# Kernel optimization log

Measured on AMD Instinct MI355X. Metric: run time of the kernel, lower is better.

## Reference

```python
import jax, jax.numpy as jnp
import numpy as np

DIM = 1024
HEADS = 16
DIM_HEAD = 64
INNER = HEADS * DIM_HEAD  # 1024
FF_INNER = 4 * DIM        # 4096
EPS = 1e-5


def _ln(t, gamma):
    mu = jnp.mean(t, axis=-1, keepdims=True)
    var = jnp.var(t, axis=-1, keepdims=True)
    return (t - mu) * jax.lax.rsqrt(var + EPS) * gamma


def setup_inputs() -> dict:
    key = jax.random.key(0)
    ks = jax.random.split(key, 8)
    B, N = 4, 1024
    s = 0.02
    return {
        "x": jax.random.normal(ks[0], (B, N, DIM), dtype=jnp.float32),
        "y": jax.random.normal(ks[1], (B, N, DIM), dtype=jnp.float32),
        "g1": jnp.ones((DIM,), dtype=jnp.float32),
        "g2": jnp.ones((DIM,), dtype=jnp.float32),
        "g_out": jnp.ones((DIM,), dtype=jnp.float32),
        "Wq": jax.random.normal(ks[2], (DIM, INNER), dtype=jnp.float32) * s,
        "Wkv": jax.random.normal(ks[3], (DIM, 2 * DIM_HEAD), dtype=jnp.float32) * s,
        "Wo": jax.random.normal(ks[4], (INNER, DIM), dtype=jnp.float32) * s,
        "Wff1": jax.random.normal(ks[5], (DIM, 2 * FF_INNER), dtype=jnp.float32) * s,
        "Wff2": jax.random.normal(ks[6], (FF_INNER, DIM), dtype=jnp.float32) * s,
    }


def reference(x, y, g1, g2, g_out, Wq, Wkv, Wo, Wff1, Wff2):
    B, N, _ = x.shape
    scale = DIM_HEAD ** -0.5
    xn = _ln(x, g1)
    yn = _ln(y, g2)  # note: torch code rebinds y = norm2(y); residual & FF use normed y
    # multi-query attention: per-head queries, single shared k/v head
    q = (xn @ Wq).reshape(B, N, HEADS, DIM_HEAD).transpose(0, 2, 1, 3) * scale  # b h n d
    kv = yn @ Wkv  # b j (2d)
    k, v = kv[..., :DIM_HEAD], kv[..., DIM_HEAD:]
    sim = jnp.einsum('bhid,bjd->bhij', q, k)
    attn = jax.nn.softmax(sim, axis=-1)  # torch code subtracts amax then softmax; identical math
    out = jnp.einsum('bhij,bjd->bhid', attn, v)
    out = out.transpose(0, 2, 1, 3).reshape(B, N, INNER)
    out = out @ Wo
    out = _ln(out + yn, g_out)
    # SwiGLU FFN on normed y: first half is value, second half is gate
    h = yn @ Wff1
    val, gate = h[..., :FF_INNER], h[..., FF_INNER:]
    ff = (jax.nn.silu(gate) * val) @ Wff2
    return out + ff
```

## Files before the change

kernel.cpp:

```cpp
#include <hip/hip_runtime.h>
#include <hip/hip_bf16.h>


typedef __attribute__((ext_vector_type(8))) short bf16x8;
typedef __attribute__((ext_vector_type(4))) short s16x4;
typedef __attribute__((ext_vector_type(4))) float f32x4;

__device__ __forceinline__ short f2b(float f) {
  union { float f; unsigned u; } v; v.f = f;
  unsigned r = (v.u + 0x7fffu + ((v.u >> 16) & 1u)) >> 16;
  return (short)r;
}

__device__ __forceinline__ void gload16(const short* g, short* l) {
  __builtin_amdgcn_global_load_lds(
      (const __attribute__((address_space(1))) void*)g,
      (__attribute__((address_space(3))) void*)l, 16, 0, 0);
}

__global__ __launch_bounds__(256) void cvtT_kernel(const float* __restrict__ in,
                                                   short* __restrict__ out,
                                                   int K, int N) {
  __shared__ float tile[32][33];
  int n0 = blockIdx.x * 32, k0 = blockIdx.y * 32;
  int tx = threadIdx.x & 7, ty = threadIdx.x >> 3;
  float4 v = *(const float4*)&in[(size_t)(k0 + ty) * N + n0 + tx * 4];
  tile[ty][tx * 4 + 0] = v.x;
  tile[ty][tx * 4 + 1] = v.y;
  tile[ty][tx * 4 + 2] = v.z;
  tile[ty][tx * 4 + 3] = v.w;
  __syncthreads();
  s16x4 o = { f2b(tile[tx * 4 + 0][ty]), f2b(tile[tx * 4 + 1][ty]),
              f2b(tile[tx * 4 + 2][ty]), f2b(tile[tx * 4 + 3][ty]) };
  *(s16x4*)&out[(size_t)(n0 + ty) * K + k0 + tx * 4] = o;
}

__global__ __launch_bounds__(256) void ln_kernel(const float* __restrict__ in,
                                                 const float* __restrict__ gamma,
                                                 short* __restrict__ out16,
                                                 float* __restrict__ out32) {
  int row = blockIdx.x;
  int t = threadIdx.x;
  float4 v = ((const float4*)(in + (size_t)row * 1024))[t];
  float s  = v.x + v.y + v.z + v.w;
  float sq = v.x*v.x + v.y*v.y + v.z*v.z + v.w*v.w;
  __shared__ float ssum[256], ssq[256];
  ssum[t] = s; ssq[t] = sq;
  __syncthreads();
  for (int o = 128; o > 0; o >>= 1) {
    if (t < o) { ssum[t] += ssum[t + o]; ssq[t] += ssq[t + o]; }
    __syncthreads();
  }
  float mu  = ssum[0] * (1.0f / 1024.0f);
  float var = ssq[0] * (1.0f / 1024.0f) - mu * mu;
  float rs  = rsqrtf(var + 1e-5f);
  float4 g = ((const float4*)gamma)[t];
  float o0 = (v.x - mu) * rs * g.x;
  float o1 = (v.y - mu) * rs * g.y;
  float o2 = (v.z - mu) * rs * g.z;
  float o3 = (v.w - mu) * rs * g.w;
  if (out16) {
    s16x4 o = { f2b(o0), f2b(o1), f2b(o2), f2b(o3) };
    ((s16x4*)out16)[(size_t)row * 256 + t] = o;
  }
  if (out32) {
    float4 o = { o0, o1, o2, o3 };
    ((float4*)out32)[(size_t)row * 256 + t] = o;
  }
}

template<int EPI, bool DUAL, int BM, int BN>
__global__ __launch_bounds__(256, 2) void gemm_ring(
    const short* __restrict__ A, const short* __restrict__ B,
    int M, int N, int Kstride, int Klen,
    short* __restrict__ out16, float* __restrict__ out32,
    const float* __restrict__ res, float scale)
{
  constexpr int DEPTH = DUAL ? 3 : 4;
  constexpr int FM = BM / 32;
  constexpr int FN = BN / 32;
  constexpr int AL = BM / 64;
  constexpr int BL = BN / 64;
  constexpr int LPT = AL + BL * (DUAL ? 2 : 1);
  __shared__ __align__(16) short As[DEPTH][BM * 32];
  __shared__ __align__(16) short Bs[DEPTH][BN * 32];
  __shared__ __align__(16) short Bs2[DUAL ? DEPTH : 1][DUAL ? BN * 32 : 8];

  int t = threadIdx.x;
  int lane = t & 63, wave = t >> 6;
  int wm = wave >> 1, wn = wave & 1;
  int lrow = lane & 15, lgrp = lane >> 4;
  int m0 = blockIdx.y * BM, n0 = blockIdx.x * BN;
  int kbase = blockIdx.z * Klen;

  int srow = lane >> 2, scol = (lane & 3) * 8;
  const short* gA  = A + (size_t)(m0 + wave * 16 + srow) * Kstride + kbase + scol;
  const short* gB  = B + (size_t)(n0 + wave * 16 + srow) * Kstride + kbase + scol;
  const short* gB2 = DUAL ? B + (size_t)(4096 + n0 + wave * 16 + srow) * Kstride + kbase + scol : gB;

  auto STAGE = [&](int slot, int kt) {
    int k0 = kt * 32;
#pragma unroll
    for (int i = 0; i < AL; i++)
      gload16(gA + (size_t)(i * 64) * Kstride + k0, &As[slot][(i * 4 + wave) * 512]);
#pragma unroll
    for (int j = 0; j < BL; j++)
      gload16(gB + (size_t)(j * 64) * Kstride + k0, &Bs[slot][(j * 4 + wave) * 512]);
    if constexpr (DUAL) {
#pragma unroll
      for (int j = 0; j < BL; j++)
        gload16(gB2 + (size_t)(j * 64) * Kstride + k0, &Bs2[slot][(j * 4 + wave) * 512]);
    }
  };

  f32x4 acc[FM][FN];
  f32x4 acc2[DUAL ? FM : 1][DUAL ? FN : 1];
  const f32x4 zero = { 0.f, 0.f, 0.f, 0.f };
#pragma unroll
  for (int i = 0; i < FM; i++)
#pragma unroll
    for (int j = 0; j < FN; j++) { acc[i][j] = zero; if (DUAL) acc2[i][j] = zero; }

  int nt = Klen / 32;
#pragma unroll
  for (int p = 0; p < DEPTH - 1; p++) STAGE(p, p);

  int slot = 0, stage_slot = DEPTH - 1;
  for (int tI = 0; tI < nt; ++tI) {
    int rem = nt - 1 - tI;
    if constexpr (DUAL) {
      if (rem >= 1) asm volatile("s_waitcnt vmcnt(6)" ::: "memory");
      else          asm volatile("s_waitcnt vmcnt(0)" ::: "memory");
    } else if constexpr (LPT == 4) {
      if (rem >= 2)      asm volatile("s_waitcnt vmcnt(8)" ::: "memory");
      else if (rem == 1) asm volatile("s_waitcnt vmcnt(4)" ::: "memory");
      else               asm volatile("s_waitcnt vmcnt(0)" ::: "memory");
    } else {
      if (rem >= 2)      asm volatile("s_waitcnt vmcnt(6)" ::: "memory");
      else if (rem == 1) asm volatile("s_waitcnt vmcnt(3)" ::: "memory");
      else               asm volatile("s_waitcnt vmcnt(0)" ::: "memory");
    }
    __builtin_amdgcn_s_barrier();
    __builtin_amdgcn_sched_barrier(0);

    if (tI + DEPTH - 1 < nt) STAGE(stage_slot, tI + DEPTH - 1);

    bf16x8 af[FM], bfr[FN], bfr2[DUAL ? FN : 1];
#pragma unroll
    for (int mf = 0; mf < FM; mf++)
      af[mf] = *(const bf16x8*)&As[slot][(wm * (BM / 2) + mf * 16 + lrow) * 32 + lgrp * 8];
#pragma unroll
    for (int nf = 0; nf < FN; nf++)
      bfr[nf] = *(const bf16x8*)&Bs[slot][(wn * (BN / 2) + nf * 16 + lrow) * 32 + lgrp * 8];
    if constexpr (DUAL) {
#pragma unroll
      for (int nf = 0; nf < FN; nf++)
        bfr2[nf] = *(const bf16x8*)&Bs2[slot][(wn * (BN / 2) + nf * 16 + lrow) * 32 + lgrp * 8];
    }

    __builtin_amdgcn_s_setprio(1);
#pragma unroll
    for (int mf = 0; mf < FM; mf++)
#pragma unroll
      for (int nf = 0; nf < FN; nf++) {
        acc[mf][nf] = __builtin_amdgcn_mfma_f32_16x16x32_bf16(af[mf], bfr[nf], acc[mf][nf], 0, 0, 0);
        if constexpr (DUAL)
          acc2[mf][nf] = __builtin_amdgcn_mfma_f32_16x16x32_bf16(af[mf], bfr2[nf], acc2[mf][nf], 0, 0, 0);
      }
    __builtin_amdgcn_s_setprio(0);

    slot = (slot + 1 == DEPTH) ? 0 : slot + 1;
    stage_slot = (stage_slot + 1 == DEPTH) ? 0 : stage_slot + 1;
  }

#pragma unroll
  for (int mf = 0; mf < FM; mf++)
#pragma unroll
    for (int nf = 0; nf < FN; nf++)
#pragma unroll
      for (int r = 0; r < 4; r++) {
        int row = m0 + wm * (BM / 2) + mf * 16 + lgrp * 4 + r;
        int col = n0 + wn * (BN / 2) + nf * 16 + lrow;
        float v = acc[mf][nf][r];
        if (EPI == 0) {
          out16[(size_t)row * N + col] = f2b(v * scale);
        } else if (EPI == 1) {
          out32[(size_t)row * N + col] = v + res[(size_t)row * N + col];
        } else if (EPI == 3) {
          out32[(size_t)blockIdx.z * M * N + (size_t)row * N + col] = v;
        } else {
          float gate = acc2[mf][nf][r];
          float sig = 1.0f / (1.0f + __expf(-gate));
          out16[(size_t)row * N + col] = f2b(v * gate * sig);
        }
      }
}

__global__ __launch_bounds__(256) void kvred_kernel(const float* __restrict__ p,
                                                    short* __restrict__ out, int n4) {
  int i = blockIdx.x * 256 + threadIdx.x;
  if (i >= n4) return;
  const int S = 4096 * 128 / 4;
  float4 a = ((const float4*)p)[i];
  float4 b = ((const float4*)p)[i + S];
  float4 c = ((const float4*)p)[i + 2 * S];
  float4 d = ((const float4*)p)[i + 3 * S];
  s16x4 o = { f2b(a.x + b.x + c.x + d.x), f2b(a.y + b.y + c.y + d.y),
              f2b(a.z + b.z + c.z + d.z), f2b(a.w + b.w + c.w + d.w) };
  ((s16x4*)out)[i] = o;
}

__global__ __launch_bounds__(256) void attn_kernel(const short* __restrict__ q,
                                                   const short* __restrict__ kv,
                                                   short* __restrict__ ao)
{
  __shared__ __align__(16) short Ks[64 * 64];
  __shared__ __align__(16) short Vs[64 * 64];
  __shared__ __align__(16) short Ps[4][32 * 64];

  int t = threadIdx.x;
  int lane = t & 63, wave = t >> 6;
  int lrow = lane & 15, lgrp = lane >> 4;
  int qt = blockIdx.x;
  int b = blockIdx.y >> 2, hg = blockIdx.y & 3;
  int h = hg * 4 + wave;

  char* Kb = (char*)Ks;
  char* Vb = (char*)Vs;
  char* Pb = (char*)Ps + wave * (32 * 64 * 2);

  bf16x8 qf[2][2];
  const short* qb = q + ((size_t)(b * 1024 + qt * 32)) * 1024 + h * 64;
#pragma unroll
  for (int mf = 0; mf < 2; mf++)
#pragma unroll
    for (int kk = 0; kk < 2; kk++)
      qf[mf][kk] = *(const bf16x8*)&qb[(size_t)(mf * 16 + lrow) * 1024 + kk * 32 + lgrp * 8];

  f32x4 oacc[2][4];
  float m_[2][4], l_[2][4];
  const f32x4 zero = { 0.f, 0.f, 0.f, 0.f };
#pragma unroll
  for (int i = 0; i < 2; i++)
#pragma unroll
    for (int j = 0; j < 4; j++) { oacc[i][j] = zero; }
#pragma unroll
  for (int i = 0; i < 2; i++)
#pragma unroll
    for (int r = 0; r < 4; r++) { m_[i][r] = -3.0e38f; l_[i][r] = 0.f; }

  int4 d[4];
  {
    const short* kvb = kv + ((size_t)(b * 1024 + lane)) * 128 + wave * 32;
#pragma unroll
    for (int i = 0; i < 4; i++) d[i] = ((const int4*)kvb)[i];
  }

  for (int j0 = 0; j0 < 1024; j0 += 64) {
    __syncthreads();
    if (wave < 2) {
      int sw = (lane & 7) << 4;
#pragma unroll
      for (int i = 0; i < 4; i++)
        *(int4*)(Kb + lane * 128 + ((wave * 64 + i * 16) ^ sw)) = d[i];
    } else {
#pragma unroll
      for (int i = 0; i < 4; i++) {
        union { int4 v; short s[8]; } u; u.v = d[i];
#pragma unroll
        for (int j = 0; j < 8; j++) {
          int dd = (wave - 2) * 32 + i * 8 + j;
          *(short*)(Vb + dd * 128 + ((lane * 2) ^ ((dd & 7) << 4))) = u.s[j];
        }
      }
    }
    if (j0 + 64 < 1024) {
      const short* kvn = kv + ((size_t)(b * 1024 + j0 + 64 + lane)) * 128 + wave * 32;
#pragma unroll
      for (int i = 0; i < 4; i++) d[i] = ((const int4*)kvn)[i];
    }
    __syncthreads();

    bf16x8 kf[4][2];
#pragma unroll
    for (int nf = 0; nf < 4; nf++) {
      int row = nf * 16 + lrow, sw = (row & 7) << 4;
      kf[nf][0] = *(const bf16x8*)(Kb + row * 128 + ((lgrp * 16) ^ sw));
      kf[nf][1] = *(const bf16x8*)(Kb + row * 128 + ((64 + lgrp * 16) ^ sw));
    }
    f32x4 sacc[2][4];
#pragma unroll
    for (int i = 0; i < 2; i++)
#pragma unroll
      for (int j = 0; j < 4; j++) sacc[i][j] = zero;
    __builtin_amdgcn_s_setprio(1);
#pragma unroll
    for (int mf = 0; mf < 2; mf++)
#pragma unroll
      for (int nf = 0; nf < 4; nf++)
#pragma unroll
        for (int kk = 0; kk < 2; kk++)
          sacc[mf][nf] = __builtin_amdgcn_mfma_f32_16x16x32_bf16(qf[mf][kk], kf[nf][kk], sacc[mf][nf], 0, 0, 0);
    __builtin_amdgcn_s_setprio(0);

    float pmax[2][4];
    bool okd = true;
#pragma unroll
    for (int mf = 0; mf < 2; mf++)
#pragma unroll
      for (int r = 0; r < 4; r++) {
        float pm = fmaxf(fmaxf(sacc[mf][0][r], sacc[mf][1][r]),
                         fmaxf(sacc[mf][2][r], sacc[mf][3][r]));
        pmax[mf][r] = pm;
        okd = okd && (pm <= m_[mf][r] + 8.0f);
      }
    if (__all(okd)) {
#pragma unroll
      for (int mf = 0; mf < 2; mf++)
#pragma unroll
        for (int r = 0; r < 4; r++) {
          int row = mf * 16 + lgrp * 4 + r, sw = (row & 7) << 4;
          float al = 0.f;
#pragma unroll
          for (int nf = 0; nf < 4; nf++) {
            float p = __expf(sacc[mf][nf][r] - m_[mf][r]);
            *(short*)(Pb + row * 128 + (((nf * 16 + lrow) * 2) ^ sw)) = f2b(p);
            al += p;
          }
          l_[mf][r] += al;
        }
    } else {
#pragma unroll
      for (int mf = 0; mf < 2; mf++)
#pragma unroll
        for (int r = 0; r < 4; r++) {
          float mx = pmax[mf][r];
#pragma unroll
          for (int o = 8; o >= 1; o >>= 1) mx = fmaxf(mx, __shfl_xor(mx, o));
          float mnew = fmaxf(m_[mf][r], mx);
          float corr = __expf(m_[mf][r] - mnew);
          int row = mf * 16 + lgrp * 4 + r, sw = (row & 7) << 4;
          float al = 0.f;
#pragma unroll
          for (int nf = 0; nf < 4; nf++) {
            float p = __expf(sacc[mf][nf][r] - mnew);
            *(short*)(Pb + row * 128 + (((nf * 16 + lrow) * 2) ^ sw)) = f2b(p);
            al += p;
          }
          l_[mf][r] = l_[mf][r] * corr + al;
          m_[mf][r] = mnew;
#pragma unroll
          for (int nf = 0; nf < 4; nf++) oacc[mf][nf][r] *= corr;
        }
    }

    bf16x8 vf[4][2], pf[2][2];
#pragma unroll
    for (int nf = 0; nf < 4; nf++) {
      int row = nf * 16 + lrow, sw = (row & 7) << 4;
      vf[nf][0] = *(const bf16x8*)(Vb + row * 128 + ((lgrp * 16) ^ sw));
      vf[nf][1] = *(const bf16x8*)(Vb + row * 128 + ((64 + lgrp * 16) ^ sw));
    }
#pragma unroll
    for (int mf = 0; mf < 2; mf++) {
      int row = mf * 16 + lrow, sw = (row & 7) << 4;
      pf[mf][0] = *(const bf16x8*)(Pb + row * 128 + ((lgrp * 16) ^ sw));
      pf[mf][1] = *(const bf16x8*)(Pb + row * 128 + ((64 + lgrp * 16) ^ sw));
    }
    __builtin_amdgcn_s_setprio(1);
#pragma unroll
    for (int mf = 0; mf < 2; mf++)
#pragma unroll
      for (int nf = 0; nf < 4; nf++)
#pragma unroll
        for (int kk = 0; kk < 2; kk++)
          oacc[mf][nf] = __builtin_amdgcn_mfma_f32_16x16x32_bf16(pf[mf][kk], vf[nf][kk], oacc[mf][nf], 0, 0, 0);
    __builtin_amdgcn_s_setprio(0);
  }

#pragma unroll
  for (int mf = 0; mf < 2; mf++)
#pragma unroll
    for (int r = 0; r < 4; r++) {
      float ls = l_[mf][r];
#pragma unroll
      for (int o = 8; o >= 1; o >>= 1) ls += __shfl_xor(ls, o);
      float inv = 1.0f / ls;
      int qrow = qt * 32 + mf * 16 + lgrp * 4 + r;
#pragma unroll
      for (int nf = 0; nf < 4; nf++) {
        float val = oacc[mf][nf][r] * inv;
        ao[((size_t)(b * 1024 + qrow)) * 1024 + h * 64 + nf * 16 + lrow] = f2b(val);
      }
    }
}

extern "C" void kernel_launch(void* const* d_in, const int* in_sizes, int n_in,
                              void* d_out, int out_size, void* d_ws, size_t ws_size,
                              hipStream_t stream) {
  const float* x     = (const float*)d_in[0];
  const float* y     = (const float*)d_in[1];
  const float* g1    = (const float*)d_in[2];
  const float* g2    = (const float*)d_in[3];
  const float* g_out = (const float*)d_in[4];
  const float* Wq    = (const float*)d_in[5];
  const float* Wkv   = (const float*)d_in[6];
  const float* Wo    = (const float*)d_in[7];
  const float* Wff1  = (const float*)d_in[8];
  const float* Wff2  = (const float*)d_in[9];

  char* ws = (char*)d_ws;
  size_t off = 0;
  auto alloc = [&](size_t bytes) { char* p = ws + off; off += bytes; return p; };
  short* wqT    = (short*)alloc((size_t)1024 * 1024 * 2);
  short* wkvT   = (short*)alloc((size_t)128 * 1024 * 2);
  short* woT    = (short*)alloc((size_t)1024 * 1024 * 2);
  short* wff1T  = (short*)alloc((size_t)8192 * 1024 * 2);
  short* wff2T  = (short*)alloc((size_t)1024 * 4096 * 2);
  short* xn16   = (short*)alloc((size_t)4096 * 1024 * 2);
  short* yn16   = (short*)alloc((size_t)4096 * 1024 * 2);
  float* ynf    = (float*)alloc((size_t)4096 * 1024 * 4);
  short* q16    = (short*)alloc((size_t)4096 * 1024 * 2);
  short* kv16   = (short*)alloc((size_t)4096 * 128 * 2);
  short* ao16   = (short*)alloc((size_t)4096 * 1024 * 2);
  float* lnout  = (float*)alloc((size_t)4096 * 1024 * 4);
  short* act16  = (short*)alloc((size_t)4096 * 4096 * 2);
  float* kvpart = (float*)alloc((size_t)4 * 4096 * 128 * 4);
  float* outf   = (float*)d_out;

  cvtT_kernel<<<dim3(1024 / 32, 1024 / 32), 256, 0, stream>>>(Wq,   wqT,   1024, 1024);
  cvtT_kernel<<<dim3(128 / 32, 1024 / 32),  256, 0, stream>>>(Wkv,  wkvT,  1024, 128);
  cvtT_kernel<<<dim3(1024 / 32, 1024 / 32), 256, 0, stream>>>(Wo,   woT,   1024, 1024);
  cvtT_kernel<<<dim3(8192 / 32, 1024 / 32), 256, 0, stream>>>(Wff1, wff1T, 1024, 8192);
  cvtT_kernel<<<dim3(1024 / 32, 4096 / 32), 256, 0, stream>>>(Wff2, wff2T, 4096, 1024);

  ln_kernel<<<4096, 256, 0, stream>>>(x, g1, xn16, nullptr);
  ln_kernel<<<4096, 256, 0, stream>>>(y, g2, yn16, ynf);

  gemm_ring<0, false, 64, 128><<<dim3(8, 64), 256, 0, stream>>>(
      xn16, wqT, 4096, 1024, 1024, 1024, q16, nullptr, nullptr, 0.125f);
  gemm_ring<3, false, 64, 128><<<dim3(1, 64, 4), 256, 0, stream>>>(
      yn16, wkvT, 4096, 128, 1024, 256, nullptr, kvpart, nullptr, 1.0f);
  kvred_kernel<<<512, 256, 0, stream>>>(kvpart, kv16, 4096 * 128 / 4);

  attn_kernel<<<dim3(32, 16), 256, 0, stream>>>(q16, kv16, ao16);

  gemm_ring<1, false, 64, 128><<<dim3(8, 64), 256, 0, stream>>>(
      ao16, woT, 4096, 1024, 1024, 1024, nullptr, outf, ynf, 1.0f);

  ln_kernel<<<4096, 256, 0, stream>>>(outf, g_out, nullptr, lnout);

  gemm_ring<2, true, 128, 128><<<dim3(32, 32), 256, 0, stream>>>(
      yn16, wff1T, 4096, 4096, 1024, 1024, act16, nullptr, nullptr, 1.0f);

  gemm_ring<1, false, 64, 128><<<dim3(8, 64), 256, 0, stream>>>(
      act16, wff2T, 4096, 1024, 4096, 4096, nullptr, outf, lnout, 1.0f);
}
```

Before: 325.4 us.

## Add dedicated 8-wave SwiGLU FF1 GEMM with interleaved prefetch phases

Replaces the dual-B templated GEMM path for the SwiGLU FF1 projection with a dedicated kernel. It uses 512 threads, a 256x128 tile with separate value and gate B buffers, and a 4-deep ring. Each k-step is split into four barrier-separated MFMA phases, with global-to-LDS prefetches spread across the phases to overlap loads with compute. The dual path is removed from the generic GEMM template. The extra barriers add synchronization overhead, and the larger tile and accumulator count raise register pressure.

New measurement: 324.6 us. About the same (-0.3%).

```diff
diff --git a/kernel.cpp b/kernel.cpp
--- a/kernel.cpp
+++ b/kernel.cpp
@@ -69,22 +69,20 @@
   }
 }
 
-template<int EPI, bool DUAL, int BM, int BN>
+template<int EPI, int BM, int BN>
 __global__ __launch_bounds__(256, 2) void gemm_ring(
     const short* __restrict__ A, const short* __restrict__ B,
     int M, int N, int Kstride, int Klen,
     short* __restrict__ out16, float* __restrict__ out32,
     const float* __restrict__ res, float scale)
 {
-  constexpr int DEPTH = DUAL ? 3 : 4;
+  constexpr int DEPTH = 4;
   constexpr int FM = BM / 32;
   constexpr int FN = BN / 32;
   constexpr int AL = BM / 64;
   constexpr int BL = BN / 64;
-  constexpr int LPT = AL + BL * (DUAL ? 2 : 1);
   __shared__ __align__(16) short As[DEPTH][BM * 32];
   __shared__ __align__(16) short Bs[DEPTH][BN * 32];
-  __shared__ __align__(16) short Bs2[DUAL ? DEPTH : 1][DUAL ? BN * 32 : 8];
 
   int t = threadIdx.x;
   int lane = t & 63, wave = t >> 6;
@@ -94,9 +92,8 @@
   int kbase = blockIdx.z * Klen;
 
   int srow = lane >> 2, scol = (lane & 3) * 8;
-  const short* gA  = A + (size_t)(m0 + wave * 16 + srow) * Kstride + kbase + scol;
-  const short* gB  = B + (size_t)(n0 + wave * 16 + srow) * Kstride + kbase + scol;
-  const short* gB2 = DUAL ? B + (size_t)(4096 + n0 + wave * 16 + srow) * Kstride + kbase + scol : gB;
+  const short* gA = A + (size_t)(m0 + wave * 16 + srow) * Kstride + kbase + scol;
+  const short* gB = B + (size_t)(n0 + wave * 16 + srow) * Kstride + kbase + scol;
 
   auto STAGE = [&](int slot, int kt) {
     int k0 = kt * 32;
@@ -106,20 +103,14 @@
 #pragma unroll
     for (int j = 0; j < BL; j++)
       gload16(gB + (size_t)(j * 64) * Kstride + k0, &Bs[slot][(j * 4 + wave) * 512]);
-    if constexpr (DUAL) {
-#pragma unroll
-      for (int j = 0; j < BL; j++)
-        gload16(gB2 + (size_t)(j * 64) * Kstride + k0, &Bs2[slot][(j * 4 + wave) * 512]);
-    }
   };
 
   f32x4 acc[FM][FN];
-  f32x4 acc2[DUAL ? FM : 1][DUAL ? FN : 1];
   const f32x4 zero = { 0.f, 0.f, 0.f, 0.f };
 #pragma unroll
   for (int i = 0; i < FM; i++)
 #pragma unroll
-    for (int j = 0; j < FN; j++) { acc[i][j] = zero; if (DUAL) acc2[i][j] = zero; }
+    for (int j = 0; j < FN; j++) acc[i][j] = zero;
 
   int nt = Klen / 32;
 #pragma unroll
@@ -128,10 +119,7 @@
   int slot = 0, stage_slot = DEPTH - 1;
   for (int tI = 0; tI < nt; ++tI) {
     int rem = nt - 1 - tI;
-    if constexpr (DUAL) {
-      if (rem >= 1) asm volatile("s_waitcnt vmcnt(6)" ::: "memory");
-      else          asm volatile("s_waitcnt vmcnt(0)" ::: "memory");
-    } else if constexpr (LPT == 4) {
+    if constexpr (AL + BL == 4) {
       if (rem >= 2)      asm volatile("s_waitcnt vmcnt(8)" ::: "memory");
       else if (rem == 1) asm volatile("s_waitcnt vmcnt(4)" ::: "memory");
       else               asm volatile("s_waitcnt vmcnt(0)" ::: "memory");
@@ -145,28 +133,20 @@
 
     if (tI + DEPTH - 1 < nt) STAGE(stage_slot, tI + DEPTH - 1);
 
-    bf16x8 af[FM], bfr[FN], bfr2[DUAL ? FN : 1];
+    bf16x8 af[FM], bfr[FN];
 #pragma unroll
     for (int mf = 0; mf < FM; mf++)
       af[mf] = *(const bf16x8*)&As[slot][(wm * (BM / 2) + mf * 16 + lrow) * 32 + lgrp * 8];
 #pragma unroll
     for (int nf = 0; nf < FN; nf++)
       bfr[nf] = *(const bf16x8*)&Bs[slot][(wn * (BN / 2) + nf * 16 + lrow) * 32 + lgrp * 8];
-    if constexpr (DUAL) {
+
+    __builtin_amdgcn_s_setprio(1);
+#pragma unroll
+    for (int mf = 0; mf < FM; mf++)
 #pragma unroll
       for (int nf = 0; nf < FN; nf++)
-        bfr2[nf] = *(const bf16x8*)&Bs2[slot][(wn * (BN / 2) + nf * 16 + lrow) * 32 + lgrp * 8];
-    }
-
-    __builtin_amdgcn_s_setprio(1);
-#pragma unroll
-    for (int mf = 0; mf < FM; mf++)
-#pragma unroll
-      for (int nf = 0; nf < FN; nf++) {
         acc[mf][nf] = __builtin_amdgcn_mfma_f32_16x16x32_bf16(af[mf], bfr[nf], acc[mf][nf], 0, 0, 0);
-        if constexpr (DUAL)
-          acc2[mf][nf] = __builtin_amdgcn_mfma_f32_16x16x32_bf16(af[mf], bfr2[nf], acc2[mf][nf], 0, 0, 0);
-      }
     __builtin_amdgcn_s_setprio(0);
 
     slot = (slot + 1 == DEPTH) ? 0 : slot + 1;
@@ -186,13 +166,132 @@
           out16[(size_t)row * N + col] = f2b(v * scale);
         } else if (EPI == 1) {
           out32[(size_t)row * N + col] = v + res[(size_t)row * N + col];
-        } else if (EPI == 3) {
+        } else {
           out32[(size_t)blockIdx.z * M * N + (size_t)row * N + col] = v;
-        } else {
-          float gate = acc2[mf][nf][r];
-          float sig = 1.0f / (1.0f + __expf(-gate));
-          out16[(size_t)row * N + col] = f2b(v * gate * sig);
         }
+      }
+}
+
+__global__ __launch_bounds__(512, 2) void gemm_ff1(
+    const short* __restrict__ A, const short* __restrict__ B,
+    short* __restrict__ out16)
+{
+  constexpr int K = 1024, NT = 32;
+  __shared__ __align__(16) short As[4][256 * 32];
+  __shared__ __align__(16) short Bv[4][128 * 32];
+  __shared__ __align__(16) short Bg[4][128 * 32];
+
+  int t = threadIdx.x;
+  int lane = t & 63, wave = t >> 6;
+  int wm = wave >> 1, wn = wave & 1;
+  int lrow = lane & 15, lgrp = lane >> 4;
+  int m0 = blockIdx.y * 256, n0 = blockIdx.x * 128;
+
+  int srow = lane >> 2, scol = (lane & 3) * 8;
+  const short* gA  = A + (size_t)(m0 + wave * 16 + srow) * K + scol;
+  const short* gBv = B + (size_t)(n0 + wave * 16 + srow) * K + scol;
+  const short* gBg = B + (size_t)(4096 + n0 + wave * 16 + srow) * K + scol;
+
+  f32x4 acc[4][4], acc2[4][4];
+  const f32x4 zero = { 0.f, 0.f, 0.f, 0.f };
+#pragma unroll
+  for (int i = 0; i < 4; i++)
+#pragma unroll
+    for (int j = 0; j < 4; j++) { acc[i][j] = zero; acc2[i][j] = zero; }
+
+#pragma unroll
+  for (int p = 0; p < 3; p++) {
+    gload16(gA + p * 32,                      &As[p][wave * 512]);
+    gload16(gA + (size_t)128 * K + p * 32,    &As[p][4096 + wave * 512]);
+    gload16(gBv + p * 32,                     &Bv[p][wave * 512]);
+    gload16(gBg + p * 32,                     &Bg[p][wave * 512]);
+  }
+
+  for (int tI = 0; tI < NT; ++tI) {
+    int slot = tI & 3, s3 = (tI + 3) & 3;
+    bool pf = (tI + 3 < NT);
+    int k3 = (tI + 3) * 32;
+    int rem = NT - 1 - tI;
+    if (rem >= 2)      asm volatile("s_waitcnt vmcnt(8)" ::: "memory");
+    else if (rem == 1) asm volatile("s_waitcnt vmcnt(4)" ::: "memory");
+    else               asm volatile("s_waitcnt vmcnt(0)" ::: "memory");
+    __builtin_amdgcn_s_barrier();
+    __builtin_amdgcn_sched_barrier(0);
+
+    bf16x8 af[4], bv[4], bg[4];
+#pragma unroll
+    for (int mf = 0; mf < 4; mf++)
+      af[mf] = *(const bf16x8*)&As[slot][(wm * 64 + mf * 16 + lrow) * 32 + lgrp * 8];
+    bv[0] = *(const bf16x8*)&Bv[slot][(wn * 64 + lrow) * 32 + lgrp * 8];
+    bv[1] = *(const bf16x8*)&Bv[slot][(wn * 64 + 16 + lrow) * 32 + lgrp * 8];
+    if (pf) gload16(gA + k3, &As[s3][wave * 512]);
+    __builtin_amdgcn_s_barrier();
+    __builtin_amdgcn_sched_barrier(0);
+    __builtin_amdgcn_s_setprio(1);
+#pragma unroll
+    for (int mf = 0; mf < 4; mf++) {
+      acc[mf][0] = __builtin_amdgcn_mfma_f32_16x16x32_bf16(af[mf], bv[0], acc[mf][0], 0, 0, 0);
+      acc[mf][1] = __builtin_amdgcn_mfma_f32_16x16x32_bf16(af[mf], bv[1], acc[mf][1], 0, 0, 0);
+    }
+    __builtin_amdgcn_s_setprio(0);
+    __builtin_amdgcn_s_barrier();
+    __builtin_amdgcn_sched_barrier(0);
+    bv[2] = *(const bf16x8*)&Bv[slot][(wn * 64 + 32 + lrow) * 32 + lgrp * 8];
+    bv[3] = *(const bf16x8*)&Bv[slot][(wn * 64 + 48 + lrow) * 32 + lgrp * 8];
+    if (pf) gload16(gA + (size_t)128 * K + k3, &As[s3][4096 + wave * 512]);
+    __builtin_amdgcn_s_barrier();
+    __builtin_amdgcn_sched_barrier(0);
+    __builtin_amdgcn_s_setprio(1);
+#pragma unroll
+    for (int mf = 0; mf < 4; mf++) {
+      acc[mf][2] = __builtin_amdgcn_mfma_f32_16x16x32_bf16(af[mf], bv[2], acc[mf][2], 0, 0, 0);
+      acc[mf][3] = __builtin_amdgcn_mfma_f32_16x16x32_bf16(af[mf], bv[3], acc[mf][3], 0, 0, 0);
+    }
+    __builtin_amdgcn_s_setprio(0);
+    __builtin_amdgcn_s_barrier();
+    __builtin_amdgcn_sched_barrier(0);
+    bg[0] = *(const bf16x8*)&Bg[slot][(wn * 64 + lrow) * 32 + lgrp * 8];
+    bg[1] = *(const bf16x8*)&Bg[slot][(wn * 64 + 16 + lrow) * 32 + lgrp * 8];
+    if (pf) gload16(gBv + k3, &Bv[s3][wave * 512]);
+    __builtin_amdgcn_s_barrier();
+    __builtin_amdgcn_sched_barrier(0);
+    __builtin_amdgcn_s_setprio(1);
+#pragma unroll
+    for (int mf = 0; mf < 4; mf++) {
+      acc2[mf][0] = __builtin_amdgcn_mfma_f32_16x16x32_bf16(af[mf], bg[0], acc2[mf][0], 0, 0, 0);
+      acc2[mf][1] = __builtin_amdgcn_mfma_f32_16x16x32_bf16(af[mf], bg[1], acc2[mf][1], 0, 0, 0);
+    }
+    __builtin_amdgcn_s_setprio(0);
+    __builtin_amdgcn_s_barrier();
+    __builtin_amdgcn_sched_barrier(0);
+    bg[2] = *(const bf16x8*)&Bg[slot][(wn * 64 + 32 + lrow) * 32 + lgrp * 8];
+    bg[3] = *(const bf16x8*)&Bg[slot][(wn * 64 + 48 + lrow) * 32 + lgrp * 8];
+    if (pf) gload16(gBg + k3, &Bg[s3][wave * 512]);
+    __builtin_amdgcn_s_barrier();
+    __builtin_amdgcn_sched_barrier(0);
+    __builtin_amdgcn_s_setprio(1);
+#pragma unroll
+    for (int mf = 0; mf < 4; mf++) {
+      acc2[mf][2] = __builtin_amdgcn_mfma_f32_16x16x32_bf16(af[mf], bg[2], acc2[mf][2], 0, 0, 0);
+      acc2[mf][3] = __builtin_amdgcn_mfma_f32_16x16x32_bf16(af[mf], bg[3], acc2[mf][3], 0, 0, 0);
+    }
+    __builtin_amdgcn_s_setprio(0);
+    __builtin_amdgcn_s_barrier();
+    __builtin_amdgcn_sched_barrier(0);
+  }
+
+#pragma unroll
+  for (int mf = 0; mf < 4; mf++)
+#pragma unroll
+    for (int nf = 0; nf < 4; nf++)
+#pragma unroll
+      for (int r = 0; r < 4; r++) {
+        int row = m0 + wm * 64 + mf * 16 + lgrp * 4 + r;
+        int col = n0 + wn * 64 + nf * 16 + lrow;
+        float v = acc[mf][nf][r];
+        float gate = acc2[mf][nf][r];
+        float sig = 1.0f / (1.0f + __expf(-gate));
+        out16[(size_t)row * 4096 + col] = f2b(v * gate * sig);
       }
 }
 
@@ -354,7 +453,7 @@
         }
     }
 
-    bf16x8 vf[4][2], pf[2][2];
+    bf16x8 vf[4][2], pfr[2][2];
 #pragma unroll
     for (int nf = 0; nf < 4; nf++) {
       int row = nf * 16 + lrow, sw = (row & 7) << 4;
@@ -364,8 +463,8 @@
 #pragma unroll
     for (int mf = 0; mf < 2; mf++) {
       int row = mf * 16 + lrow, sw = (row & 7) << 4;
-      pf[mf][0] = *(const bf16x8*)(Pb + row * 128 + ((lgrp * 16) ^ sw));
-      pf[mf][1] = *(const bf16x8*)(Pb + row * 128 + ((64 + lgrp * 16) ^ sw));
+      pfr[mf][0] = *(const bf16x8*)(Pb + row * 128 + ((lgrp * 16) ^ sw));
+      pfr[mf][1] = *(const bf16x8*)(Pb + row * 128 + ((64 + lgrp * 16) ^ sw));
     }
     __builtin_amdgcn_s_setprio(1);
 #pragma unroll
@@ -374,7 +473,7 @@
       for (int nf = 0; nf < 4; nf++)
 #pragma unroll
         for (int kk = 0; kk < 2; kk++)
-          oacc[mf][nf] = __builtin_amdgcn_mfma_f32_16x16x32_bf16(pf[mf][kk], vf[nf][kk], oacc[mf][nf], 0, 0, 0);
+          oacc[mf][nf] = __builtin_amdgcn_mfma_f32_16x16x32_bf16(pfr[mf][kk], vf[nf][kk], oacc[mf][nf], 0, 0, 0);
     __builtin_amdgcn_s_setprio(0);
   }
 
@@ -437,22 +536,21 @@
   ln_kernel<<<4096, 256, 0, stream>>>(x, g1, xn16, nullptr);
   ln_kernel<<<4096, 256, 0, stream>>>(y, g2, yn16, ynf);
 
-  gemm_ring<0, false, 64, 128><<<dim3(8, 64), 256, 0, stream>>>(
+  gemm_ring<0, 64, 128><<<dim3(8, 64), 256, 0, stream>>>(
       xn16, wqT, 4096, 1024, 1024, 1024, q16, nullptr, nullptr, 0.125f);
-  gemm_ring<3, false, 64, 128><<<dim3(1, 64, 4), 256, 0, stream>>>(
+  gemm_ring<3, 64, 128><<<dim3(1, 64, 4), 256, 0, stream>>>(
       yn16, wkvT, 4096, 128, 1024, 256, nullptr, kvpart, nullptr, 1.0f);
   kvred_kernel<<<512, 256, 0, stream>>>(kvpart, kv16, 4096 * 128 / 4);
 
   attn_kernel<<<dim3(32, 16), 256, 0, stream>>>(q16, kv16, ao16);
 
-  gemm_ring<1, false, 64, 128><<<dim3(8, 64), 256, 0, stream>>>(
+  gemm_ring<1, 64, 128><<<dim3(8, 64), 256, 0, stream>>>(
       ao16, woT, 4096, 1024, 1024, 1024, nullptr, outf, ynf, 1.0f);
 
   ln_kernel<<<4096, 256, 0, stream>>>(outf, g_out, nullptr, lnout);
 
-  gemm_ring<2, true, 128, 128><<<dim3(32, 32), 256, 0, stream>>>(
-      yn16, wff1T, 4096, 4096, 1024, 1024, act16, nullptr, nullptr, 1.0f);
-
-  gemm_ring<1, false, 64, 128><<<dim3(8, 64), 256, 0, stream>>>(
+  gemm_ff1<<<dim3(32, 16), 512, 0, stream>>>(yn16, wff1T, act16);
+
+  gemm_ring<1, 64, 128><<<dim3(8, 64), 256, 0, stream>>>(
       act16, wff2T, 4096, 1024, 4096, 4096, nullptr, outf, lnout, 1.0f);
 }
```
